# Performance work log

Measured on AMD Instinct MI355X. Metric: run time of the kernel, lower is better.

The kernel has to match this reference:

```python
import jax, jax.numpy as jnp
import numpy as np

T_DATA = 20000
E_NO = 2000
I_NO = 500
SUB = 12
T_SYN = 200
T_HIST = 100
SB = 3   # syn_basis_no
HB = 3   # hist_basis_no
PB = 3   # prop_basis_no


def setup_inputs() -> dict:
    key = jax.random.key(0)
    ks = jax.random.split(key, 20)
    f32 = jnp.float32
    S_e = (jax.random.uniform(ks[0], (T_DATA, E_NO)) < 0.05).astype(f32)
    S_i = (jax.random.uniform(ks[1], (T_DATA, I_NO)) < 0.05).astype(f32)
    C_syn_e = (jax.random.uniform(ks[2], (SUB, E_NO)) < 1.0 / SUB).astype(f32)
    C_syn_i = (jax.random.uniform(ks[3], (SUB, I_NO)) < 1.0 / SUB).astype(f32)
    # dendritic adjacency: strictly lower-triangular-ish sparse connectivity
    C_den = (jax.random.uniform(ks[4], (SUB, SUB)) < 0.15).astype(f32) * jnp.tril(jnp.ones((SUB, SUB), f32), -1)
    return {
        'S_e': S_e, 'S_i': S_i,
        'C_syn_e': C_syn_e, 'C_syn_i': C_syn_i, 'C_den': C_den,
        'W_s_syn': jax.random.normal(ks[5], (SUB, SB, 2), f32) * 0.04,
        'W_ns_syn': jax.random.normal(ks[6], (SUB, SB, 2), f32) * 0.02,
        'Delta_s_syn': jax.random.uniform(ks[7], (SUB, 2), f32),
        'Delta_ns_syn': jax.random.uniform(ks[8], (SUB, 2), f32),
        'Theta_s': jnp.zeros((SUB,), f32),
        'Theta_ns': jnp.zeros((SUB,), f32),
        'W_s_sub': jax.random.uniform(ks[9], (SUB,), f32),
        'W_ns_sub': jax.random.uniform(ks[10], (SUB,), f32),
        'W_s_hist': jax.random.uniform(ks[11], (SUB - 1, HB), f32) * -0.04,
        'W_ns_hist': jax.random.uniform(ks[12], (SUB - 1, HB), f32) * -0.02,
        'W_s_prop': jax.random.uniform(ks[13], (SUB, PB), f32) * 0.04,
        'W_ns_prop': jax.random.uniform(ks[14], (SUB, PB), f32) * 0.02,
    }


def _syn_kernels(W, Delta):
    # W: [sub, SB, 2], Delta: [sub, 2] -> kern [sub, 2, T_SYN]
    t = jnp.arange(T_SYN, dtype=jnp.float32)
    ts = jnp.maximum(t[None, None, :] - jnp.exp(Delta)[:, :, None], 0.0)  # [sub,2,T]
    tau = jnp.exp(jnp.arange(SB, dtype=jnp.float32) * 0.5)                # Tau = arange(0, SB*0.5, 0.5)
    tt = ts[:, None, :, :] / tau[None, :, None, None]                     # [sub,SB,2,T]
    return jnp.einsum('sbct,sbc->sct', tt * jnp.exp(-tt), W)


def _decay_kernels(W, T, nb):
    # W: [n, nb] -> kern [n, T]; tau_b = exp(0.5*b)
    t = jnp.arange(T, dtype=jnp.float32)
    tau = jnp.exp(jnp.arange(nb, dtype=jnp.float32) * 0.5)
    tt = t[None, :] / tau[:, None]  # [nb, T]
    return jnp.einsum('bt,sb->st', tt * jnp.exp(-tt), W)


def _causal_conv(x, kern):
    # x: [T, C], kern: [C, K]; out[t, c] = sum_k kern[c, k] * x[t-k, c]
    C, K = kern.shape
    y = jax.lax.conv_general_dilated(
        x.T[None], kern[:, None, ::-1], (1,), [(K - 1, 0)],
        feature_group_count=C, dimension_numbers=('NCW', 'OIW', 'NCW'))
    return y[0].T


def reference(S_e, S_i, C_syn_e, C_syn_i, C_den, W_s_syn, W_ns_syn,
              Delta_s_syn, Delta_ns_syn, Theta_s, Theta_ns,
              W_s_sub, W_ns_sub, W_s_hist, W_ns_hist, W_s_prop, W_ns_prop):
    sub = C_den.shape[0]
    # --- synaptic kernels + causal filtering (vectorized over subunits) ---
    k_s = _syn_kernels(W_s_syn, Delta_s_syn)      # [sub,2,T_SYN]
    k_ns = _syn_kernels(W_ns_syn, Delta_ns_syn)
    IN_e = S_e @ C_syn_e.T                        # [T, sub]
    IN_i = S_i @ C_syn_i.T
    syn_s_in = _causal_conv(IN_e, k_s[:, 0]) + _causal_conv(IN_i, k_s[:, 1])    # [T, sub]
    syn_ns_in = _causal_conv(IN_e, k_ns[:, 0]) + _causal_conv(IN_i, k_ns[:, 1])
    # --- history / propagation kernels ---
    hist_s = _decay_kernels(W_s_hist, T_HIST, HB)   # [sub-1, T_HIST]
    hist_ns = _decay_kernels(W_ns_hist, T_HIST, HB)
    prop_s = _decay_kernels(W_s_prop, T_HIST, PB)   # [sub, T_HIST]
    prop_ns = _decay_kernels(W_ns_prop, T_HIST, PB)
    # Z_pad (spike history buffer) stays zero in this forward, so the filtered
    # hist/prop terms are identically zero; keep the computation for fidelity.
    z0 = jnp.zeros((sub - 1, T_HIST), syn_s_in.dtype)
    filt_s_hist = (hist_s * z0).sum(-1)      # [sub-1]
    filt_ns_hist = (hist_ns * z0).sum(-1)
    sp0 = C_den[:, 1:] @ z0                   # [sub, T_HIST]
    filt_s_prop = (prop_s * sp0).sum(-1)      # [sub]
    filt_ns_prop = (prop_ns * sp0).sum(-1)

    def step(carry, syn_t):
        Y_s, Y_ns = carry
        s_t, ns_t = syn_t
        X_s = s_t + filt_s_prop + C_den @ Y_s + Theta_s
        X_s = X_s.at[1:].add(filt_s_hist)
        X_ns = ns_t + filt_ns_prop + C_den @ Y_ns + Theta_ns
        X_ns = X_ns.at[1:].add(filt_ns_hist)
        X_ns_out = jax.nn.sigmoid(X_ns)
        Y_ns_n = X_ns_out * W_ns_sub
        sig_s = jax.nn.sigmoid(X_s)
        Y_s_n = jnp.concatenate([sig_s[:1] * W_s_sub[:1], X_ns_out[1:] * W_s_sub[1:]])
        # per-step output: [Y_s(t+1), Y_ns(t+1), spike probs of non-root subunits]
        return (Y_s_n, Y_ns_n), jnp.concatenate([Y_s_n, Y_ns_n, sig_s[1:]])

    init = (jnp.zeros((sub,), syn_s_in.dtype), jnp.zeros((sub,), syn_s_in.dtype))
    _, out = jax.lax.scan(step, init, (syn_s_in, syn_ns_in))
    return out  # [T_DATA, 3*sub - 1]


if __name__ == '__main__':
    inp = setup_inputs()
    o = reference(**inp)
    print(o.shape)
```

## Files before the change

kernel.cpp:

```cpp
#include <hip/hip_runtime.h>

typedef unsigned int uint;
typedef unsigned long long u64;

#define TD 20000
#define WS_H      0
#define WS_SPREAD 9600
#define WS_IN     14600
#define WS_SYN    494600

__device__ __forceinline__ float sigf(float x) { return 1.f / (1.f + __expf(-x)); }

__global__ __launch_bounds__(256) void k1_precomp(
    const float* __restrict__ Ce, const float* __restrict__ Ci,
    const float* __restrict__ Wsy_s, const float* __restrict__ Wsy_ns,
    const float* __restrict__ Del_s, const float* __restrict__ Del_ns,
    float* __restrict__ ws) {
  int p = blockIdx.x * 256 + threadIdx.x;
  if (p < 2400) {
    int k = p / 12, s = p - (p / 12) * 12;
    float o[4];
    for (int ch = 0; ch < 2; ++ch) {
      const float* W = ch ? Wsy_ns : Wsy_s;
      const float* D = ch ? Del_ns : Del_s;
      for (int c = 0; c < 2; ++c) {
        float ts = fmaxf((float)k - __expf(D[s * 2 + c]), 0.f);
        float v = 0.f;
        for (int b = 0; b < 3; ++b) {
          float tt = ts * __expf(-0.5f * (float)b);
          v += W[s * 6 + b * 2 + c] * tt * __expf(-tt);
        }
        o[ch * 2 + c] = v;
      }
    }
    float* H = ws + WS_H + (size_t)(k * 12 + s) * 4;
    H[0] = o[0]; H[1] = o[1]; H[2] = o[2]; H[3] = o[3];
  }
  int q = p - 2400;
  if (q >= 0 && q < 2500) {
    uint m = 0;
    if (q < 2000) {
      for (int s = 0; s < 12; ++s) m |= (Ce[s * 2000 + q] != 0.f ? (1u << s) : 0u);
    } else {
      int e = q - 2000;
      for (int s = 0; s < 12; ++s) m |= (Ci[s * 500 + e] != 0.f ? (1u << s) : 0u);
    }
    u64 sp = 0ull;
    for (int s = 0; s < 12; ++s) sp |= (u64)((m >> s) & 1u) << (5 * s);
    ((uint2*)(ws + WS_SPREAD))[q] = make_uint2((uint)sp, (uint)(sp >> 32));
  }
}

__global__ __launch_bounds__(256) void k2_project(
    const float* __restrict__ Se, const float* __restrict__ Si,
    float* __restrict__ ws) {
  __shared__ __align__(16) uint2 sp[2500];
  {
    const uint2* g = (const uint2*)(ws + WS_SPREAD);
    for (int p = threadIdx.x; p < 2500; p += 256) sp[p] = g[p];
  }
  __syncthreads();
  const int lane = threadIdx.x & 63;
  const int t = blockIdx.x * 4 + (threadIdx.x >> 6);
  const uint4* SP4 = (const uint4*)sp;
  float* INb = ws + WS_IN;

  uint eTot[12];
#pragma unroll
  for (int s = 0; s < 12; ++s) eTot[s] = 0u;
  u64 acc = 0ull;
  const float4* Sr = (const float4*)(Se + (size_t)t * 2000);
#pragma unroll
  for (int it = 0; it < 8; ++it) {
    int i4 = lane + it * 64;
    if (i4 < 500) {
      float4 sv = Sr[i4];
      uint4 a = SP4[2 * i4];
      uint4 b = SP4[2 * i4 + 1];
      u64 m0 = (u64)a.x | ((u64)a.y << 32);
      u64 m1 = (u64)a.z | ((u64)a.w << 32);
      u64 m2 = (u64)b.x | ((u64)b.y << 32);
      u64 m3 = (u64)b.z | ((u64)b.w << 32);
      acc += (sv.x != 0.f ? m0 : 0ull);
      acc += (sv.y != 0.f ? m1 : 0ull);
      acc += (sv.z != 0.f ? m2 : 0ull);
      acc += (sv.w != 0.f ? m3 : 0ull);
    }
    if (it == 3) {
#pragma unroll
      for (int s = 0; s < 12; ++s) eTot[s] += (uint)(acc >> (5 * s)) & 31u;
      acc = 0ull;
    }
  }
#pragma unroll
  for (int s = 0; s < 12; ++s) eTot[s] += (uint)(acc >> (5 * s)) & 31u;
  u64 accI = 0ull;
  const float4* Sir = (const float4*)(Si + (size_t)t * 500);
#pragma unroll
  for (int it = 0; it < 2; ++it) {
    int i4 = lane + it * 64;
    if (i4 < 125) {
      float4 sv = Sir[i4];
      uint4 a = SP4[1000 + 2 * i4];
      uint4 b = SP4[1000 + 2 * i4 + 1];
      u64 m0 = (u64)a.x | ((u64)a.y << 32);
      u64 m1 = (u64)a.z | ((u64)a.w << 32);
      u64 m2 = (u64)b.x | ((u64)b.y << 32);
      u64 m3 = (u64)b.z | ((u64)b.w << 32);
      accI += (sv.x != 0.f ? m0 : 0ull);
      accI += (sv.y != 0.f ? m1 : 0ull);
      accI += (sv.z != 0.f ? m2 : 0ull);
      accI += (sv.w != 0.f ? m3 : 0ull);
    }
  }
  uint pk[12];
#pragma unroll
  for (int s = 0; s < 12; ++s)
    pk[s] = eTot[s] | (((uint)(accI >> (5 * s)) & 31u) << 16);
#pragma unroll
  for (int s = 0; s < 12; ++s) {
    uint v = pk[s];
    v += __shfl_xor(v, 32, 64);
    v += __shfl_xor(v, 16, 64);
    v += __shfl_xor(v, 8, 64);
    v += __shfl_xor(v, 4, 64);
    v += __shfl_xor(v, 2, 64);
    v += __shfl_xor(v, 1, 64);
    pk[s] = v;
  }
  if (lane == 0) {
    float4* o = (float4*)(INb + (size_t)t * 24);
    o[0] = make_float4((float)(pk[0] & 0xffffu), (float)(pk[1] & 0xffffu),
                       (float)(pk[2] & 0xffffu), (float)(pk[3] & 0xffffu));
    o[1] = make_float4((float)(pk[4] & 0xffffu), (float)(pk[5] & 0xffffu),
                       (float)(pk[6] & 0xffffu), (float)(pk[7] & 0xffffu));
    o[2] = make_float4((float)(pk[8] & 0xffffu), (float)(pk[9] & 0xffffu),
                       (float)(pk[10] & 0xffffu), (float)(pk[11] & 0xffffu));
    o[3] = make_float4((float)(pk[0] >> 16), (float)(pk[1] >> 16),
                       (float)(pk[2] >> 16), (float)(pk[3] >> 16));
    o[4] = make_float4((float)(pk[4] >> 16), (float)(pk[5] >> 16),
                       (float)(pk[6] >> 16), (float)(pk[7] >> 16));
    o[5] = make_float4((float)(pk[8] >> 16), (float)(pk[9] >> 16),
                       (float)(pk[10] >> 16), (float)(pk[11] >> 16));
  }
}

__global__ __launch_bounds__(256) void k3_conv(float* __restrict__ ws) {
  __shared__ float tile[6 * 264];
  __shared__ float red[4 * 64 * 7];
  const int g = blockIdx.y;
  const int t0 = blockIdx.x * 64;
  const float* INb = ws + WS_IN;
  for (int p = threadIdx.x; p < 263 * 6; p += 256) {
    int row = p / 6, c = p - row * 6;
    int ch = (c < 3) ? (3 * g + c) : (9 + 3 * g + c);
    int gt = t0 - 199 + row;
    tile[c * 264 + row] = (gt >= 0 && gt < TD) ? INb[(size_t)gt * 24 + ch] : 0.f;
  }
  __syncthreads();
  const int lane = threadIdx.x & 63;
  const int q = threadIdx.x >> 6;
  const float4* H4 = (const float4*)(ws + WS_H);
  float accs[3] = {0.f, 0.f, 0.f}, accn[3] = {0.f, 0.f, 0.f};
  for (int kk = 0; kk < 25; ++kk) {
    int k = q * 50 + kk * 2;
    int rb = lane + 198 - k;
#pragma unroll
    for (int s = 0; s < 3; ++s) {
      float ve0 = tile[s * 264 + rb];
      float ve1 = tile[s * 264 + rb + 1];
      float vi0 = tile[(3 + s) * 264 + rb];
      float vi1 = tile[(3 + s) * 264 + rb + 1];
      float4 h0 = H4[k * 12 + 3 * g + s];
      float4 h1 = H4[(k + 1) * 12 + 3 * g + s];
      accs[s] += h0.x * ve1 + h0.y * vi1 + h1.x * ve0 + h1.y * vi0;
      accn[s] += h0.z * ve1 + h0.w * vi1 + h1.z * ve0 + h1.w * vi0;
    }
  }
  float* mr = red + (q * 64 + lane) * 7;
#pragma unroll
  for (int s = 0; s < 3; ++s) { mr[s] = accs[s]; mr[3 + s] = accn[s]; }
  __syncthreads();
  for (int p = threadIdx.x; p < 64 * 6; p += 256) {
    int row = p / 6, c = p - row * 6;
    if (t0 + row < TD) {
      float sum = red[row * 7 + c] + red[(64 + row) * 7 + c] +
                  red[(128 + row) * 7 + c] + red[(192 + row) * 7 + c];
      int ch = (c < 3) ? (3 * g + c) : (9 + 3 * g + c);
      ws[WS_SYN + (size_t)(t0 + row) * 24 + ch] = sum;
    }
  }
}

__global__ void k45_out(
    const float* __restrict__ Cden, const float* __restrict__ Ws_sub,
    const float* __restrict__ Wns_sub, const float* __restrict__ Th_s,
    const float* __restrict__ Th_ns, const float* __restrict__ ws,
    float* __restrict__ out) {
  __shared__ float lout[64 * 35];
  const int t = blockIdx.x * 64 + threadIdx.x;
  float v[35];
#pragma unroll
  for (int m = 0; m < 35; ++m) v[m] = 0.f;
  if (t < TD) {
    const float* SYN = ws + WS_SYN;
    float dns[12][12];
#pragma unroll
    for (int i = 1; i < 12; ++i)
#pragma unroll
      for (int j = 0; j < i; ++j) dns[i][j] = Cden[i * 12 + j] * Wns_sub[j];
    float th[12];
#pragma unroll
    for (int i = 0; i < 12; ++i) th[i] = Th_ns[i];
    float ap[12], an[12];
#pragma unroll
    for (int i = 0; i < 12; ++i) { ap[i] = 0.f; an[i] = 0.f; }
    int start = t - 12; if (start < 0) start = 0;
    for (int tau = start; tau <= t; ++tau) {
      const float4* sr = (const float4*)(SYN + (size_t)tau * 24 + 12);
      float4 s0 = sr[0], s1 = sr[1], s2 = sr[2];
      float sn[12] = {s0.x, s0.y, s0.z, s0.w, s1.x, s1.y, s1.z, s1.w,
                      s2.x, s2.y, s2.z, s2.w};
#pragma unroll
      for (int i = 0; i < 12; ++i) {
        float x = sn[i] + th[i];
#pragma unroll
        for (int j = 0; j < i; ++j) x += dns[i][j] * ap[j];
        an[i] = sigf(x);
      }
      if (tau < t) {
#pragma unroll
        for (int i = 0; i < 12; ++i) ap[i] = an[i];
      }
    }
    float sns[12];
    {
      const float4* sr = (const float4*)(SYN + (size_t)t * 24);
      float4 s0 = sr[0], s1 = sr[1], s2 = sr[2];
      sns[0] = s0.x; sns[1] = s0.y; sns[2] = s0.z; sns[3] = s0.w;
      sns[4] = s1.x; sns[5] = s1.y; sns[6] = s1.z; sns[7] = s1.w;
      sns[8] = s2.x; sns[9] = s2.y; sns[10] = s2.z; sns[11] = s2.w;
    }
    float carry[12];
    carry[0] = (t > 0) ? Ws_sub[0] * sigf(SYN[(size_t)(t - 1) * 24] + Th_s[0]) : 0.f;
#pragma unroll
    for (int j = 1; j < 12; ++j) carry[j] = Ws_sub[j] * ap[j];
    float B[12];
#pragma unroll
    for (int i = 0; i < 12; ++i) {
      float x = sns[i] + Th_s[i];
#pragma unroll
      for (int j = 0; j < i; ++j) x += Cden[i * 12 + j] * carry[j];
      B[i] = sigf(x);
    }
    v[0] = B[0] * Ws_sub[0];
#pragma unroll
    for (int i = 1; i < 12; ++i) v[i] = an[i] * Ws_sub[i];
#pragma unroll
    for (int i = 0; i < 12; ++i) v[12 + i] = an[i] * Wns_sub[i];
#pragma unroll
    for (int i = 1; i < 12; ++i) v[23 + i] = B[i];
  }
#pragma unroll
  for (int m = 0; m < 35; ++m) lout[threadIdx.x * 35 + m] = v[m];
  __syncthreads();
  const int t0 = blockIdx.x * 64;
  int nrow = TD - t0; if (nrow > 64) nrow = 64;
  const int valid = nrow * 35;
  for (int p = threadIdx.x; p < valid; p += 64) out[(size_t)t0 * 35 + p] = lout[p];
}

extern "C" void kernel_launch(void* const* d_in, const int* in_sizes, int n_in,
                              void* d_out, int out_size, void* d_ws, size_t ws_size,
                              hipStream_t stream) {
  const float* Se = (const float*)d_in[0];
  const float* Si = (const float*)d_in[1];
  const float* Ce = (const float*)d_in[2];
  const float* Ci = (const float*)d_in[3];
  const float* Cden = (const float*)d_in[4];
  const float* Wsy_s = (const float*)d_in[5];
  const float* Wsy_ns = (const float*)d_in[6];
  const float* Del_s = (const float*)d_in[7];
  const float* Del_ns = (const float*)d_in[8];
  const float* Th_s = (const float*)d_in[9];
  const float* Th_ns = (const float*)d_in[10];
  const float* Ws_sub = (const float*)d_in[11];
  const float* Wns_sub = (const float*)d_in[12];
  float* ws = (float*)d_ws;
  float* out = (float*)d_out;

  k1_precomp<<<20, 256, 0, stream>>>(Ce, Ci, Wsy_s, Wsy_ns, Del_s, Del_ns, ws);
  k2_project<<<5000, 256, 0, stream>>>(Se, Si, ws);
  dim3 g3(313, 4);
  k3_conv<<<g3, 256, 0, stream>>>(ws);
  k45_out<<<313, 64, 0, stream>>>(Cden, Ws_sub, Wns_sub, Th_s, Th_ns, ws, out);
}
```

Measured before the change: 329.1 us.

## Process two time rows per wave in projection, read mask table from global

Result: faster. 304.3 us, median of 2 (-7.6%).

```diff
diff --git a/kernel.cpp b/kernel.cpp
--- a/kernel.cpp
+++ b/kernel.cpp
@@ -2,6 +2,7 @@
 
 typedef unsigned int uint;
 typedef unsigned long long u64;
+typedef float f32x4 __attribute__((ext_vector_type(4)));
 
 #define TD 20000
 #define WS_H      0
@@ -47,101 +48,139 @@
     }
     u64 sp = 0ull;
     for (int s = 0; s < 12; ++s) sp |= (u64)((m >> s) & 1u) << (5 * s);
-    ((uint2*)(ws + WS_SPREAD))[q] = make_uint2((uint)sp, (uint)(sp >> 32));
+    uint lo = (uint)sp, hi = (uint)(sp >> 32);
+    uint* U = (uint*)(ws + WS_SPREAD);
+    int base, idx;
+    if (q < 2000) {
+      int g4 = q >> 2, r = q & 3;
+      base = (r < 2) ? 0 : 2000;
+      idx = g4 * 4 + 2 * (r & 1);
+    } else {
+      int e = q - 2000;
+      int g4 = e >> 2, r = e & 3;
+      base = (r < 2) ? 4000 : 4500;
+      idx = g4 * 4 + 2 * (r & 1);
+    }
+    U[base + idx] = lo;
+    U[base + idx + 1] = hi;
   }
 }
 
 __global__ __launch_bounds__(256) void k2_project(
     const float* __restrict__ Se, const float* __restrict__ Si,
     float* __restrict__ ws) {
-  __shared__ __align__(16) uint2 sp[2500];
-  {
-    const uint2* g = (const uint2*)(ws + WS_SPREAD);
-    for (int p = threadIdx.x; p < 2500; p += 256) sp[p] = g[p];
-  }
-  __syncthreads();
   const int lane = threadIdx.x & 63;
-  const int t = blockIdx.x * 4 + (threadIdx.x >> 6);
-  const uint4* SP4 = (const uint4*)sp;
+  const int w = blockIdx.x * 4 + (threadIdx.x >> 6);
+  const size_t t0 = (size_t)w * 2;
+  const uint4* U4 = (const uint4*)(ws + WS_SPREAD);
   float* INb = ws + WS_IN;
 
-  uint eTot[12];
-#pragma unroll
-  for (int s = 0; s < 12; ++s) eTot[s] = 0u;
-  u64 acc = 0ull;
-  const float4* Sr = (const float4*)(Se + (size_t)t * 2000);
+  uint e0[12], e1[12];
+#pragma unroll
+  for (int s = 0; s < 12; ++s) { e0[s] = 0u; e1[s] = 0u; }
+  u64 a0 = 0ull, a1 = 0ull;
+  const f32x4* S0 = (const f32x4*)(Se + t0 * 2000);
+  const f32x4* S1 = S0 + 500;
 #pragma unroll
   for (int it = 0; it < 8; ++it) {
     int i4 = lane + it * 64;
     if (i4 < 500) {
-      float4 sv = Sr[i4];
-      uint4 a = SP4[2 * i4];
-      uint4 b = SP4[2 * i4 + 1];
+      uint4 a = U4[i4];
+      uint4 b = U4[500 + i4];
       u64 m0 = (u64)a.x | ((u64)a.y << 32);
       u64 m1 = (u64)a.z | ((u64)a.w << 32);
       u64 m2 = (u64)b.x | ((u64)b.y << 32);
       u64 m3 = (u64)b.z | ((u64)b.w << 32);
-      acc += (sv.x != 0.f ? m0 : 0ull);
-      acc += (sv.y != 0.f ? m1 : 0ull);
-      acc += (sv.z != 0.f ? m2 : 0ull);
-      acc += (sv.w != 0.f ? m3 : 0ull);
+      f32x4 v0 = __builtin_nontemporal_load(&S0[i4]);
+      f32x4 v1 = __builtin_nontemporal_load(&S1[i4]);
+      a0 += (v0.x != 0.f ? m0 : 0ull); a1 += (v1.x != 0.f ? m0 : 0ull);
+      a0 += (v0.y != 0.f ? m1 : 0ull); a1 += (v1.y != 0.f ? m1 : 0ull);
+      a0 += (v0.z != 0.f ? m2 : 0ull); a1 += (v1.z != 0.f ? m2 : 0ull);
+      a0 += (v0.w != 0.f ? m3 : 0ull); a1 += (v1.w != 0.f ? m3 : 0ull);
     }
     if (it == 3) {
 #pragma unroll
-      for (int s = 0; s < 12; ++s) eTot[s] += (uint)(acc >> (5 * s)) & 31u;
-      acc = 0ull;
-    }
-  }
-#pragma unroll
-  for (int s = 0; s < 12; ++s) eTot[s] += (uint)(acc >> (5 * s)) & 31u;
-  u64 accI = 0ull;
-  const float4* Sir = (const float4*)(Si + (size_t)t * 500);
+      for (int s = 0; s < 12; ++s) {
+        e0[s] += (uint)(a0 >> (5 * s)) & 31u;
+        e1[s] += (uint)(a1 >> (5 * s)) & 31u;
+      }
+      a0 = 0ull; a1 = 0ull;
+    }
+  }
+#pragma unroll
+  for (int s = 0; s < 12; ++s) {
+    e0[s] += (uint)(a0 >> (5 * s)) & 31u;
+    e1[s] += (uint)(a1 >> (5 * s)) & 31u;
+  }
+  u64 ai0 = 0ull, ai1 = 0ull;
+  const f32x4* T0 = (const f32x4*)(Si + t0 * 500);
+  const f32x4* T1 = T0 + 125;
 #pragma unroll
   for (int it = 0; it < 2; ++it) {
     int i4 = lane + it * 64;
     if (i4 < 125) {
-      float4 sv = Sir[i4];
-      uint4 a = SP4[1000 + 2 * i4];
-      uint4 b = SP4[1000 + 2 * i4 + 1];
+      uint4 a = U4[1000 + i4];
+      uint4 b = U4[1125 + i4];
       u64 m0 = (u64)a.x | ((u64)a.y << 32);
       u64 m1 = (u64)a.z | ((u64)a.w << 32);
       u64 m2 = (u64)b.x | ((u64)b.y << 32);
       u64 m3 = (u64)b.z | ((u64)b.w << 32);
-      accI += (sv.x != 0.f ? m0 : 0ull);
-      accI += (sv.y != 0.f ? m1 : 0ull);
-      accI += (sv.z != 0.f ? m2 : 0ull);
-      accI += (sv.w != 0.f ? m3 : 0ull);
-    }
-  }
-  uint pk[12];
-#pragma unroll
-  for (int s = 0; s < 12; ++s)
-    pk[s] = eTot[s] | (((uint)(accI >> (5 * s)) & 31u) << 16);
+      f32x4 v0 = __builtin_nontemporal_load(&T0[i4]);
+      f32x4 v1 = __builtin_nontemporal_load(&T1[i4]);
+      ai0 += (v0.x != 0.f ? m0 : 0ull); ai1 += (v1.x != 0.f ? m0 : 0ull);
+      ai0 += (v0.y != 0.f ? m1 : 0ull); ai1 += (v1.y != 0.f ? m1 : 0ull);
+      ai0 += (v0.z != 0.f ? m2 : 0ull); ai1 += (v1.z != 0.f ? m2 : 0ull);
+      ai0 += (v0.w != 0.f ? m3 : 0ull); ai1 += (v1.w != 0.f ? m3 : 0ull);
+    }
+  }
+  uint p0[12], p1[12];
 #pragma unroll
   for (int s = 0; s < 12; ++s) {
-    uint v = pk[s];
-    v += __shfl_xor(v, 32, 64);
-    v += __shfl_xor(v, 16, 64);
-    v += __shfl_xor(v, 8, 64);
-    v += __shfl_xor(v, 4, 64);
-    v += __shfl_xor(v, 2, 64);
-    v += __shfl_xor(v, 1, 64);
-    pk[s] = v;
+    p0[s] = e0[s] | (((uint)(ai0 >> (5 * s)) & 31u) << 16);
+    p1[s] = e1[s] | (((uint)(ai1 >> (5 * s)) & 31u) << 16);
+  }
+#pragma unroll
+  for (int s = 0; s < 12; ++s) {
+    uint v = p0[s];
+    v += __shfl_xor(v, 32, 64); v += __shfl_xor(v, 16, 64);
+    v += __shfl_xor(v, 8, 64);  v += __shfl_xor(v, 4, 64);
+    v += __shfl_xor(v, 2, 64);  v += __shfl_xor(v, 1, 64);
+    p0[s] = v;
+    uint u = p1[s];
+    u += __shfl_xor(u, 32, 64); u += __shfl_xor(u, 16, 64);
+    u += __shfl_xor(u, 8, 64);  u += __shfl_xor(u, 4, 64);
+    u += __shfl_xor(u, 2, 64);  u += __shfl_xor(u, 1, 64);
+    p1[s] = u;
   }
   if (lane == 0) {
-    float4* o = (float4*)(INb + (size_t)t * 24);
-    o[0] = make_float4((float)(pk[0] & 0xffffu), (float)(pk[1] & 0xffffu),
-                       (float)(pk[2] & 0xffffu), (float)(pk[3] & 0xffffu));
-    o[1] = make_float4((float)(pk[4] & 0xffffu), (float)(pk[5] & 0xffffu),
-                       (float)(pk[6] & 0xffffu), (float)(pk[7] & 0xffffu));
-    o[2] = make_float4((float)(pk[8] & 0xffffu), (float)(pk[9] & 0xffffu),
-                       (float)(pk[10] & 0xffffu), (float)(pk[11] & 0xffffu));
-    o[3] = make_float4((float)(pk[0] >> 16), (float)(pk[1] >> 16),
-                       (float)(pk[2] >> 16), (float)(pk[3] >> 16));
-    o[4] = make_float4((float)(pk[4] >> 16), (float)(pk[5] >> 16),
-                       (float)(pk[6] >> 16), (float)(pk[7] >> 16));
-    o[5] = make_float4((float)(pk[8] >> 16), (float)(pk[9] >> 16),
-                       (float)(pk[10] >> 16), (float)(pk[11] >> 16));
+    float4* o = (float4*)(INb + t0 * 24);
+    o[0] = make_float4((float)(p0[0] & 0xffffu), (float)(p0[1] & 0xffffu),
+                       (float)(p0[2] & 0xffffu), (float)(p0[3] & 0xffffu));
+    o[1] = make_float4((float)(p0[4] & 0xffffu), (float)(p0[5] & 0xffffu),
+                       (float)(p0[6] & 0xffffu), (float)(p0[7] & 0xffffu));
+    o[2] = make_float4((float)(p0[8] & 0xffffu), (float)(p0[9] & 0xffffu),
+                       (float)(p0[10] & 0xffffu), (float)(p0[11] & 0xffffu));
+    o[3] = make_float4((float)(p0[0] >> 16), (float)(p0[1] >> 16),
+                       (float)(p0[2] >> 16), (float)(p0[3] >> 16));
+    o[4] = make_float4((float)(p0[4] >> 16), (float)(p0[5] >> 16),
+                       (float)(p0[6] >> 16), (float)(p0[7] >> 16));
+    o[5] = make_float4((float)(p0[8] >> 16), (float)(p0[9] >> 16),
+                       (float)(p0[10] >> 16), (float)(p0[11] >> 16));
+  }
+  if (lane == 1) {
+    float4* o = (float4*)(INb + (t0 + 1) * 24);
+    o[0] = make_float4((float)(p1[0] & 0xffffu), (float)(p1[1] & 0xffffu),
+                       (float)(p1[2] & 0xffffu), (float)(p1[3] & 0xffffu));
+    o[1] = make_float4((float)(p1[4] & 0xffffu), (float)(p1[5] & 0xffffu),
+                       (float)(p1[6] & 0xffffu), (float)(p1[7] & 0xffffu));
+    o[2] = make_float4((float)(p1[8] & 0xffffu), (float)(p1[9] & 0xffffu),
+                       (float)(p1[10] & 0xffffu), (float)(p1[11] & 0xffffu));
+    o[3] = make_float4((float)(p1[0] >> 16), (float)(p1[1] >> 16),
+                       (float)(p1[2] >> 16), (float)(p1[3] >> 16));
+    o[4] = make_float4((float)(p1[4] >> 16), (float)(p1[5] >> 16),
+                       (float)(p1[6] >> 16), (float)(p1[7] >> 16));
+    o[5] = make_float4((float)(p1[8] >> 16), (float)(p1[9] >> 16),
+                       (float)(p1[10] >> 16), (float)(p1[11] >> 16));
   }
 }
 
@@ -161,9 +200,10 @@
   const int lane = threadIdx.x & 63;
   const int q = threadIdx.x >> 6;
   const float4* H4 = (const float4*)(ws + WS_H);
+  const int gs = 3 * g;
   float accs[3] = {0.f, 0.f, 0.f}, accn[3] = {0.f, 0.f, 0.f};
   for (int kk = 0; kk < 25; ++kk) {
-    int k = q * 50 + kk * 2;
+    int k = __builtin_amdgcn_readfirstlane(q * 50 + kk * 2);
     int rb = lane + 198 - k;
 #pragma unroll
     for (int s = 0; s < 3; ++s) {
@@ -171,8 +211,8 @@
       float ve1 = tile[s * 264 + rb + 1];
       float vi0 = tile[(3 + s) * 264 + rb];
       float vi1 = tile[(3 + s) * 264 + rb + 1];
-      float4 h0 = H4[k * 12 + 3 * g + s];
-      float4 h1 = H4[(k + 1) * 12 + 3 * g + s];
+      float4 h0 = H4[k * 12 + gs + s];
+      float4 h1 = H4[(k + 1) * 12 + gs + s];
       accs[s] += h0.x * ve1 + h0.y * vi1 + h1.x * ve0 + h1.y * vi0;
       accn[s] += h0.z * ve1 + h0.w * vi1 + h1.z * ve0 + h1.w * vi0;
     }
@@ -290,7 +330,7 @@
   float* out = (float*)d_out;
 
   k1_precomp<<<20, 256, 0, stream>>>(Ce, Ci, Wsy_s, Wsy_ns, Del_s, Del_ns, ws);
-  k2_project<<<5000, 256, 0, stream>>>(Se, Si, ws);
+  k2_project<<<2500, 256, 0, stream>>>(Se, Si, ws);
   dim3 g3(313, 4);
   k3_conv<<<g3, 256, 0, stream>>>(ws);
   k45_out<<<313, 64, 0, stream>>>(Cden, Ws_sub, Wns_sub, Th_s, Th_ns, ws, out);
```
